# Kernel tuning notes

Hardware: AMD Instinct MI355X
Metric: run time of the kernel (lower is better)

Reference implementation:

```python
import jax, jax.numpy as jnp
import numpy as np

B, T, D, H = 2, 2048, 2048, 16
HD = D // H  # head_dim = 128
NEG = -1e9


def setup_inputs() -> dict:
    key = jax.random.key(0)
    k1, k2, k3 = jax.random.split(key, 3)
    x = jax.random.normal(k1, (B, T, D), dtype=jnp.float32)
    # additive causal mask: 0 on/below diagonal, large negative above
    mask = jnp.where(jnp.tril(jnp.ones((T, T), dtype=bool)), 0.0, NEG).astype(jnp.float32)
    causal_mask = mask[None, None]  # [1,1,T,T]
    w_qkv = jax.random.normal(k2, (3 * D, D), dtype=jnp.float32) * (D ** -0.5)
    w_out = jax.random.normal(k3, (D, D), dtype=jnp.float32) * (D ** -0.5)
    b_out = jnp.zeros((D,), dtype=jnp.float32)
    return {"x": x, "causal_mask": causal_mask, "w_qkv": w_qkv, "w_out": w_out, "b_out": b_out}


def reference(x, causal_mask, w_qkv, w_out, b_out):
    scale = HD ** -0.5
    qkv = jnp.einsum('btd,ed->bte', x, w_qkv)          # [B,T,3D]
    q, k, v = jnp.split(qkv, 3, axis=-1)
    def heads(t):  # [B,T,D] -> [B,H,T,HD]
        return t.reshape(B, T, H, HD).transpose(0, 2, 1, 3)
    q, k, v = heads(q), heads(k), heads(v)
    attn = jnp.einsum('bhqd,bhkd->bhqk', q, k) * scale + causal_mask
    attn = jax.nn.softmax(attn, axis=-1)
    out = jnp.einsum('bhqk,bhkd->bhqd', attn, v)       # [B,H,T,HD]
    out = out.transpose(0, 2, 1, 3).reshape(B, T, D)
    return jnp.einsum('btd,ed->bte', out, w_out) + b_out
```

## Files before the change

### kernel.cpp

```cpp
#include <hip/hip_runtime.h>
#include <stdint.h>

typedef uint16_t u16;
typedef __attribute__((ext_vector_type(8))) short short8;
typedef __attribute__((ext_vector_type(4))) float f32x4;
typedef __attribute__((ext_vector_type(16))) float f32x16;

#define MFMA16(a, b, c) __builtin_amdgcn_mfma_f32_16x16x32_bf16((a), (b), (c), 0, 0, 0)
#define MFMA32(a, b, c) __builtin_amdgcn_mfma_f32_32x32x16_bf16((a), (b), (c), 0, 0, 0)
#define AS1 __attribute__((address_space(1)))
#define AS3 __attribute__((address_space(3)))

__device__ __forceinline__ void gld_lds16(const u16* g, u16* l) {
  __builtin_amdgcn_global_load_lds((const AS1 void*)g, (AS3 void*)l, 16, 0, 0);
}

__device__ __forceinline__ u16 f2bf(float f) {
  uint32_t u = __float_as_uint(f);
  u += 0x7fffu + ((u >> 16) & 1u);
  return (u16)(u >> 16);
}

__global__ __launch_bounds__(256) void cvt_all(const float* __restrict__ x,
                                               const float* __restrict__ wqkv,
                                               const float* __restrict__ wout,
                                               u16* __restrict__ xb,
                                               u16* __restrict__ wqkvb,
                                               u16* __restrict__ woutb) {
  const int n1 = 8388608 / 4, n2 = 12582912 / 4;
  int i = blockIdx.x * 256 + threadIdx.x;
  const float* src;
  u16* dst;
  int j;
  if (i < n1) {
    src = x; dst = xb; j = i;
  } else if (i < n1 + n2) {
    src = wqkv; dst = wqkvb; j = i - n1;
  } else {
    src = wout; dst = woutb; j = i - n1 - n2;
  }
  float4 v = ((const float4*)src)[j];
  uint2 o;
  o.x = (uint32_t)f2bf(v.x) | ((uint32_t)f2bf(v.y) << 16);
  o.y = (uint32_t)f2bf(v.z) | ((uint32_t)f2bf(v.w) << 16);
  ((uint2*)dst)[j] = o;
}

template <int N>
__device__ __forceinline__ void bar_vm() {
  asm volatile("s_waitcnt vmcnt(%0)\n\ts_barrier" ::"n"(N) : "memory");
}

template <int MFR>
__device__ __forceinline__ void gemm_core3(const u16* __restrict__ Ab,
                                           const u16* __restrict__ Bb,
                                           u16* sm, int tid,
                                           f32x4 acc[MFR][4]) {
  constexpr int AROWS = MFR * 32;
  constexpr int ASZ = AROWS * 32;
  constexpr int BSZ = 128 * 32;
  constexpr int BUF = ASZ + BSZ;
  constexpr int NT = 64;
  constexpr int ALD = AROWS / 64;
  constexpr int VN = ALD + 2;

  const int lane = tid & 63, w = tid >> 6;
  const int wr = w >> 1, wc = w & 1;
  const int lo = lane & 15, q4 = lane >> 4;
  const int pcl = (((lo & 1) << 2) | q4) ^ ((lo >> 1) & 7);
  const int loff = (lo >> 1) * 64 + pcl * 8;

  auto stage = [&](int g) {
    u16* As = sm + (g % 3) * BUF;
    u16* Bs = As + ASZ;
    const int k0 = g * 32;
#pragma unroll
    for (int s = 0; s < ALD; ++s) {
      const int c = tid + s * 256;
      const int sr = c >> 3, pc = c & 7;
      const int t = pc ^ (sr & 7);
      const int r = sr * 2 + (t >> 2), c4 = t & 3;
      gld_lds16(Ab + (size_t)r * 2048 + k0 + c4 * 8, As + c * 8);
    }
#pragma unroll
    for (int s = 0; s < 2; ++s) {
      const int c = tid + s * 256;
      const int sr = c >> 3, pc = c & 7;
      const int t = pc ^ (sr & 7);
      const int r = sr * 2 + (t >> 2), c4 = t & 3;
      gld_lds16(Bb + (size_t)r * 2048 + k0 + c4 * 8, Bs + c * 8);
    }
  };

  stage(0);
  stage(1);
  bar_vm<VN>();

  for (int g = 0; g < NT; ++g) {
    const u16* As = sm + (g % 3) * BUF;
    const u16* Bs = As + ASZ;
    if (g + 2 < NT) stage(g + 2);
    short8 af[MFR], bf[4];
#pragma unroll
    for (int i = 0; i < MFR; ++i)
      af[i] = *(const short8*)(As + (wr * (MFR * 16) + i * 16) * 32 + loff);
#pragma unroll
    for (int j = 0; j < 4; ++j)
      bf[j] = *(const short8*)(Bs + (wc * 64 + j * 16) * 32 + loff);
    __builtin_amdgcn_s_setprio(1);
#pragma unroll
    for (int i = 0; i < MFR; ++i)
#pragma unroll
      for (int j = 0; j < 4; ++j) acc[i][j] = MFMA16(af[i], bf[j], acc[i][j]);
    __builtin_amdgcn_s_setprio(0);
    if (g + 1 < NT) {
      if (g + 2 < NT) {
        bar_vm<VN>();
      } else {
        bar_vm<0>();
      }
    }
  }
}

__global__ __launch_bounds__(256, 2) void proj_gemm(const u16* __restrict__ xb,
                                                    const u16* __restrict__ wqkvb,
                                                    u16* __restrict__ qkb,
                                                    u16* __restrict__ vtb) {
  __shared__ u16 sm[3 * (256 * 32 + 128 * 32)];
  const int tid = threadIdx.x;
  const int lane = tid & 63, w = tid >> 6;
  const int wr = w >> 1, wc = w & 1;
  const int lo = lane & 15, q4 = lane >> 4;

  if (blockIdx.x < 512) {
    int bx = blockIdx.x;
    bx = (bx & 7) * 64 + (bx >> 3);
    const int mt = bx >> 5, nt = bx & 31;
    const u16* Ab = xb + (size_t)mt * 256 * 2048;
    const u16* Bb = wqkvb + (size_t)nt * 128 * 2048;
    u16* C = qkb + (size_t)mt * 256 * 4096 + nt * 128;
    f32x4 acc[8][4];
    const f32x4 fzero = {0.f, 0.f, 0.f, 0.f};
#pragma unroll
    for (int i = 0; i < 8; ++i)
#pragma unroll
      for (int j = 0; j < 4; ++j) acc[i][j] = fzero;
    gemm_core3<8>(Ab, Bb, sm, tid, acc);
#pragma unroll
    for (int i = 0; i < 8; ++i)
#pragma unroll
      for (int j = 0; j < 4; ++j) {
        const int col = wc * 64 + j * 16 + lo;
#pragma unroll
        for (int e = 0; e < 4; ++e) {
          const int row = wr * 128 + i * 16 + q4 * 4 + e;
          C[(size_t)row * 4096 + col] = f2bf(acc[i][j][e]);
        }
      }
  } else {
    int idx = blockIdx.x - 512;
    idx = (idx & 7) * 64 + (idx >> 3);
    const int mt = idx >> 5, nt = idx & 31;
    const u16* Ab = wqkvb + (size_t)(4096 + mt * 128) * 2048;
    const u16* Bb = xb + (size_t)nt * 128 * 2048;
    u16* C = vtb + (size_t)mt * 128 * 4096 + nt * 128;
    f32x4 acc[4][4];
    const f32x4 fzero = {0.f, 0.f, 0.f, 0.f};
#pragma unroll
    for (int i = 0; i < 4; ++i)
#pragma unroll
      for (int j = 0; j < 4; ++j) acc[i][j] = fzero;
    gemm_core3<4>(Ab, Bb, sm, tid, acc);
#pragma unroll
    for (int i = 0; i < 4; ++i)
#pragma unroll
      for (int j = 0; j < 4; ++j) {
        const int col = wc * 64 + j * 16 + lo;
#pragma unroll
        for (int e = 0; e < 4; ++e) {
          const int row = wr * 64 + i * 16 + q4 * 4 + e;
          C[(size_t)row * 4096 + col] = f2bf(acc[i][j][e]);
        }
      }
  }
}

__global__ __launch_bounds__(256, 2) void out_gemm(const u16* __restrict__ A,
                                                   const u16* __restrict__ B,
                                                   float* __restrict__ Cf,
                                                   const float* __restrict__ bias) {
  __shared__ u16 sm[3 * (256 * 32 + 128 * 32)];
  int bx = blockIdx.x;
  bx = (bx & 7) * 32 + (bx >> 3);
  const int tid = threadIdx.x;
  const int mt = bx >> 4, nt = bx & 15;
  const u16* Ab = A + (size_t)mt * 256 * 2048;
  const u16* Bb = B + (size_t)nt * 128 * 2048;
  f32x4 acc[8][4];
  const f32x4 fzero = {0.f, 0.f, 0.f, 0.f};
#pragma unroll
  for (int i = 0; i < 8; ++i)
#pragma unroll
    for (int j = 0; j < 4; ++j) acc[i][j] = fzero;

  gemm_core3<8>(Ab, Bb, sm, tid, acc);

  const int lane = tid & 63, w = tid >> 6;
  const int wr = w >> 1, wc = w & 1;
  const int lo = lane & 15, q4 = lane >> 4;
#pragma unroll
  for (int i = 0; i < 8; ++i)
#pragma unroll
    for (int j = 0; j < 4; ++j) {
      const int col = nt * 128 + wc * 64 + j * 16 + lo;
      const float bv = bias[col];
#pragma unroll
      for (int e = 0; e < 4; ++e) {
        const int row = mt * 256 + wr * 128 + i * 16 + q4 * 4 + e;
        Cf[(size_t)row * 2048 + col] = acc[i][j][e] + bv;
      }
    }
}

__device__ __forceinline__ int swz(int r, int c) {
  return r * 128 + (c ^ (((r ^ (r >> 3)) & 7) << 4));
}

__global__ __launch_bounds__(512) void flash_attn(const u16* __restrict__ qk,
                                                  const u16* __restrict__ vt,
                                                  u16* __restrict__ aout) {
  constexpr int T = 2048, WQK = 4096, D = 2048;
  constexpr int TILE = 128 * 128;
  __shared__ u16 smem[5 * TILE];

  const int bx = blockIdx.x;
  const int p = bx >> 5;
  const int g = bx & 31;
  const int h = g & 15, b = g >> 4;
  const int tid = threadIdx.x, lane = tid & 63, w = tid >> 6;
  const int wr = w >> 1, wcc = w & 1;
  const int l31 = lane & 31, h5 = lane >> 5;

  const u16* Qb = qk + (size_t)b * T * WQK + h * 128;
  const u16* Kb = Qb + 2048;
  const u16* Vtb = vt + (size_t)h * 128 * 4096 + b * 2048;
  u16* Ps = smem + 4 * TILE;

  const float cexp = 0.08838834764831843f * 1.4426950408889634f;
  short8 onesf;
#pragma unroll
  for (int j = 0; j < 8; ++j) onesf[j] = (short)0x3F80;

  for (int half = 0; half < 2; ++half) {
    const int qt = half ? p : 15 - p;
    const int q0 = qt * 128;

    short8 qf[8];
#pragma unroll
    for (int kc = 0; kc < 8; ++kc)
      qf[kc] = *(const short8*)(Qb + (size_t)(q0 + wr * 32 + l31) * WQK +
                                kc * 16 + h5 * 8);

    f32x16 o[2], osum;
#pragma unroll
    for (int e = 0; e < 16; ++e) { o[0][e] = 0.f; o[1][e] = 0.f; osum[e] = 0.f; }

    __syncthreads();
#pragma unroll
    for (int s = 0; s < 4; ++s) {
      const int c = tid + s * 512, r = c >> 4, cc = c & 15;
      const int cs = cc ^ (((r ^ (r >> 3)) & 7) << 1);
      gld_lds16(Kb + (size_t)r * WQK + cs * 8, smem + c * 8);
      gld_lds16(Vtb + (size_t)r * 4096 + cs * 8, smem + 2 * TILE + c * 8);
    }

    for (int kt = 0; kt <= qt; ++kt) {
      const int curo = (kt & 1) * TILE, nxto = TILE - curo;
      __syncthreads();
      if (kt < qt) {
        const int k0n = (kt + 1) * 128;
#pragma unroll
        for (int s = 0; s < 4; ++s) {
          const int c = tid + s * 512, r = c >> 4, cc = c & 15;
          const int cs = cc ^ (((r ^ (r >> 3)) & 7) << 1);
          gld_lds16(Kb + (size_t)(k0n + r) * WQK + cs * 8, smem + nxto + c * 8);
          gld_lds16(Vtb + (size_t)r * 4096 + k0n + cs * 8,
                    smem + 2 * TILE + nxto + c * 8);
        }
      }

      const u16* Ksc = smem + curo;
      const u16* Vsc = smem + 2 * TILE + curo;

      f32x16 s2[2];
#pragma unroll
      for (int e = 0; e < 16; ++e) { s2[0][e] = 0.f; s2[1][e] = 0.f; }
#pragma unroll
      for (int kc = 0; kc < 8; ++kc)
#pragma unroll
        for (int ct = 0; ct < 2; ++ct) {
          short8 kf = *(const short8*)&Ksc[swz(wcc * 64 + ct * 32 + l31,
                                               kc * 16 + h5 * 8)];
          s2[ct] = MFMA32(qf[kc], kf, s2[ct]);
        }

      const bool diag = (kt == qt);
#pragma unroll
      for (int ct = 0; ct < 2; ++ct) {
        const int kcol = wcc * 64 + ct * 32 + l31;
#pragma unroll
        for (int reg = 0; reg < 16; ++reg) {
          const int qrow = wr * 32 + (reg & 3) + 8 * (reg >> 2) + 4 * h5;
          float pv = exp2f(s2[ct][reg] * cexp);
          if (diag && (kcol > qrow)) pv = 0.f;
          Ps[swz(qrow, kcol)] = f2bf(pv);
        }
      }
      asm volatile("s_waitcnt lgkmcnt(0)\n\ts_barrier" ::: "memory");

#pragma unroll
      for (int kc = 0; kc < 8; ++kc) {
        short8 pa = *(const short8*)&Ps[swz(wr * 32 + l31, kc * 16 + h5 * 8)];
        osum = MFMA32(pa, onesf, osum);
#pragma unroll
        for (int dt = 0; dt < 2; ++dt) {
          short8 vf = *(const short8*)&Vsc[swz(wcc * 64 + dt * 32 + l31,
                                               kc * 16 + h5 * 8)];
          o[dt] = MFMA32(pa, vf, o[dt]);
        }
      }
    }

#pragma unroll
    for (int reg = 0; reg < 16; ++reg) {
      const int row = q0 + wr * 32 + (reg & 3) + 8 * (reg >> 2) + 4 * h5;
      const float inv = 1.f / osum[reg];
#pragma unroll
      for (int dt = 0; dt < 2; ++dt)
        aout[(size_t)(b * T + row) * D + h * 128 + wcc * 64 + dt * 32 + l31] =
            f2bf(o[dt][reg] * inv);
    }
  }
}

extern "C" void kernel_launch(void* const* d_in, const int* in_sizes, int n_in,
                              void* d_out, int out_size, void* d_ws, size_t ws_size,
                              hipStream_t stream) {
  const float* x = (const float*)d_in[0];
  const float* w_qkv = (const float*)d_in[2];
  const float* w_out = (const float*)d_in[3];
  const float* b_out = (const float*)d_in[4];
  float* out = (float*)d_out;

  const int BT = 4096, D = 2048, D3 = 6144;
  u16* xb = (u16*)d_ws;
  u16* wqkvb = xb + (size_t)BT * D;
  u16* woutb = wqkvb + (size_t)D3 * D;
  u16* qkb = woutb + (size_t)D * D;
  u16* vtb = qkb + (size_t)BT * 4096;
  u16* attnb = vtb + (size_t)D * BT;

  const int total4 = (BT * D + D3 * D + D * D) / 4;
  cvt_all<<<total4 / 256, 256, 0, stream>>>(x, w_qkv, w_out, xb, wqkvb, woutb);
  proj_gemm<<<1024, 256, 0, stream>>>(xb, wqkvb, qkb, vtb);
  flash_attn<<<256, 512, 0, stream>>>(qkb, vtb, attnb);
  out_gemm<<<256, 256, 0, stream>>>(attnb, woutb, out, b_out);
}
```

Measured before the change: 366.4 us.

## Split QKV projection into 8-wave 256x256 QK GEMM and separate 256-row V GEMM

Replaces the single combined projection kernel with two launches. The Q/K part uses a new 512-thread kernel with 256x256 output tiles, a K-step of 64, double-buffered LDS and quarter-by-quarter interleaved staging of the next tile alongside the MFMAs. The V-transpose part now uses 256-row tiles in its own launch. The aim is more reuse per loaded byte and better overlap of loads with compute. The cost is an extra kernel launch and a more intricate barrier/vmcnt schedule that must be exactly right.

```diff
diff --git a/kernel.cpp b/kernel.cpp
--- a/kernel.cpp
+++ b/kernel.cpp
@@ -50,6 +50,118 @@
 __device__ __forceinline__ void bar_vm() {
   asm volatile("s_waitcnt vmcnt(%0)\n\ts_barrier" ::"n"(N) : "memory");
 }
+__device__ __forceinline__ void bar_fence() {
+  asm volatile("s_barrier" ::: "memory");
+}
+
+__global__ __launch_bounds__(512, 2) void proj8_gemm(const u16* __restrict__ xb,
+                                                     const u16* __restrict__ wqkvb,
+                                                     u16* __restrict__ qkb) {
+  constexpr int ASZ = 256 * 64;
+  constexpr int NT = 32;
+  __shared__ u16 sm[4 * ASZ];
+
+  int bx = blockIdx.x;
+  bx = (bx & 7) * 32 + (bx >> 3);
+  const int mt = bx >> 4, nt = bx & 15;
+  const u16* Ab = xb + (size_t)mt * 256 * 2048;
+  const u16* Bb = wqkvb + (size_t)nt * 256 * 2048;
+  u16* C = qkb + (size_t)mt * 256 * 4096 + nt * 256;
+
+  const int tid = threadIdx.x, lane = tid & 63, w = tid >> 6;
+  const int wm = w >> 2, wn = w & 3;
+  const int lo = lane & 15, q4 = lane >> 4;
+
+  f32x4 acc[8][4];
+  const f32x4 fzero = {0.f, 0.f, 0.f, 0.f};
+#pragma unroll
+  for (int i = 0; i < 8; ++i)
+#pragma unroll
+    for (int j = 0; j < 4; ++j) acc[i][j] = fzero;
+
+  auto stage_half = [&](int tau, int h) {
+    const int slot = tau & 1;
+    const int k0 = tau * 64;
+    const u16* G = (h < 2) ? Bb : Ab;
+    u16* L = sm + (h < 2 ? 2 * ASZ : 0) + slot * ASZ;
+#pragma unroll
+    for (int s = 0; s < 2; ++s) {
+      const int c = tid + s * 512;
+      const int hr = c >> 3, pc = c & 7;
+      const int r = (h < 2) ? (h * 128 + hr)
+                            : ((hr & 63) + ((hr >> 6) << 7) + ((h & 1) << 6));
+      const int c4 = pc ^ (r & 7);
+      gld_lds16(G + (size_t)r * 2048 + k0 + c4 * 8, L + r * 64 + pc * 8);
+    }
+  };
+
+  stage_half(0, 0);
+  stage_half(0, 1);
+  stage_half(0, 2);
+  stage_half(0, 3);
+  bar_vm<2>();
+
+  for (int tau = 0; tau < NT; ++tau) {
+    const u16* As = sm + (tau & 1) * ASZ;
+    const u16* Bs = sm + 2 * ASZ + (tau & 1) * ASZ;
+    short8 bf[8];
+#pragma unroll
+    for (int q = 0; q < 4; ++q) {
+      if (q == 0) {
+#pragma unroll
+        for (int j = 0; j < 4; ++j)
+#pragma unroll
+          for (int kk = 0; kk < 2; ++kk) {
+            const int r = wn * 64 + j * 16 + lo;
+            bf[j * 2 + kk] =
+                *(const short8*)(Bs + r * 64 + (((kk * 4 + q4) ^ (r & 7)) * 8));
+          }
+      }
+      short8 af[2][2];
+#pragma unroll
+      for (int i = 0; i < 2; ++i)
+#pragma unroll
+        for (int kk = 0; kk < 2; ++kk) {
+          const int r = wm * 128 + q * 32 + i * 16 + lo;
+          af[i][kk] =
+              *(const short8*)(As + r * 64 + (((kk * 4 + q4) ^ (r & 7)) * 8));
+        }
+      if (tau + 1 < NT) stage_half(tau + 1, q);
+      bar_fence();
+      __builtin_amdgcn_s_setprio(1);
+#pragma unroll
+      for (int i = 0; i < 2; ++i)
+#pragma unroll
+        for (int j = 0; j < 4; ++j)
+#pragma unroll
+          for (int kk = 0; kk < 2; ++kk)
+            acc[q * 2 + i][j] = MFMA16(af[i][kk], bf[j * 2 + kk], acc[q * 2 + i][j]);
+      __builtin_amdgcn_s_setprio(0);
+      if (q == 0) {
+        if (tau == NT - 1) bar_vm<0>();
+        else bar_vm<2>();
+      } else if (q == 1) {
+        bar_vm<4>();
+      } else if (q == 2) {
+        bar_vm<6>();
+      } else {
+        if (tau < NT - 1) bar_vm<2>();
+      }
+    }
+  }
+
+#pragma unroll
+  for (int i = 0; i < 8; ++i)
+#pragma unroll
+    for (int j = 0; j < 4; ++j) {
+      const int col = wn * 64 + j * 16 + lo;
+#pragma unroll
+      for (int e = 0; e < 4; ++e) {
+        const int row = wm * 128 + i * 16 + q4 * 4 + e;
+        C[(size_t)row * 4096 + col] = f2bf(acc[i][j][e]);
+      }
+    }
+}
 
 template <int MFR>
 __device__ __forceinline__ void gemm_core3(const u16* __restrict__ Ab,
@@ -123,67 +235,40 @@
   }
 }
 
-__global__ __launch_bounds__(256, 2) void proj_gemm(const u16* __restrict__ xb,
-                                                    const u16* __restrict__ wqkvb,
-                                                    u16* __restrict__ qkb,
-                                                    u16* __restrict__ vtb) {
+__global__ __launch_bounds__(256, 2) void vproj_gemm(const u16* __restrict__ wqkvb,
+                                                     const u16* __restrict__ xb,
+                                                     u16* __restrict__ vtb) {
   __shared__ u16 sm[3 * (256 * 32 + 128 * 32)];
+  int bx = blockIdx.x;
+  bx = (bx & 7) * 32 + (bx >> 3);
   const int tid = threadIdx.x;
+  const int mt = bx >> 5, nt = bx & 31;
+  const u16* Ab = wqkvb + (size_t)(4096 + mt * 256) * 2048;
+  const u16* Bb = xb + (size_t)nt * 128 * 2048;
+  u16* C = vtb + (size_t)mt * 256 * 4096 + nt * 128;
+  f32x4 acc[8][4];
+  const f32x4 fzero = {0.f, 0.f, 0.f, 0.f};
+#pragma unroll
+  for (int i = 0; i < 8; ++i)
+#pragma unroll
+    for (int j = 0; j < 4; ++j) acc[i][j] = fzero;
+
+  gemm_core3<8>(Ab, Bb, sm, tid, acc);
+
   const int lane = tid & 63, w = tid >> 6;
   const int wr = w >> 1, wc = w & 1;
   const int lo = lane & 15, q4 = lane >> 4;
-
-  if (blockIdx.x < 512) {
-    int bx = blockIdx.x;
-    bx = (bx & 7) * 64 + (bx >> 3);
-    const int mt = bx >> 5, nt = bx & 31;
-    const u16* Ab = xb + (size_t)mt * 256 * 2048;
-    const u16* Bb = wqkvb + (size_t)nt * 128 * 2048;
-    u16* C = qkb + (size_t)mt * 256 * 4096 + nt * 128;
-    f32x4 acc[8][4];
-    const f32x4 fzero = {0.f, 0.f, 0.f, 0.f};
-#pragma unroll
-    for (int i = 0; i < 8; ++i)
-#pragma unroll
-      for (int j = 0; j < 4; ++j) acc[i][j] = fzero;
-    gemm_core3<8>(Ab, Bb, sm, tid, acc);
-#pragma unroll
-    for (int i = 0; i < 8; ++i)
-#pragma unroll
-      for (int j = 0; j < 4; ++j) {
-        const int col = wc * 64 + j * 16 + lo;
-#pragma unroll
-        for (int e = 0; e < 4; ++e) {
-          const int row = wr * 128 + i * 16 + q4 * 4 + e;
-          C[(size_t)row * 4096 + col] = f2bf(acc[i][j][e]);
-        }
-      }
-  } else {
-    int idx = blockIdx.x - 512;
-    idx = (idx & 7) * 64 + (idx >> 3);
-    const int mt = idx >> 5, nt = idx & 31;
-    const u16* Ab = wqkvb + (size_t)(4096 + mt * 128) * 2048;
-    const u16* Bb = xb + (size_t)nt * 128 * 2048;
-    u16* C = vtb + (size_t)mt * 128 * 4096 + nt * 128;
-    f32x4 acc[4][4];
-    const f32x4 fzero = {0.f, 0.f, 0.f, 0.f};
-#pragma unroll
-    for (int i = 0; i < 4; ++i)
-#pragma unroll
-      for (int j = 0; j < 4; ++j) acc[i][j] = fzero;
-    gemm_core3<4>(Ab, Bb, sm, tid, acc);
-#pragma unroll
-    for (int i = 0; i < 4; ++i)
-#pragma unroll
-      for (int j = 0; j < 4; ++j) {
-        const int col = wc * 64 + j * 16 + lo;
-#pragma unroll
-        for (int e = 0; e < 4; ++e) {
-          const int row = wr * 64 + i * 16 + q4 * 4 + e;
-          C[(size_t)row * 4096 + col] = f2bf(acc[i][j][e]);
-        }
-      }
-  }
+#pragma unroll
+  for (int i = 0; i < 8; ++i)
+#pragma unroll
+    for (int j = 0; j < 4; ++j) {
+      const int col = wc * 64 + j * 16 + lo;
+#pragma unroll
+      for (int e = 0; e < 4; ++e) {
+        const int row = wr * 128 + i * 16 + q4 * 4 + e;
+        C[(size_t)row * 4096 + col] = f2bf(acc[i][j][e]);
+      }
+    }
 }
 
 __global__ __launch_bounds__(256, 2) void out_gemm(const u16* __restrict__ A,
@@ -363,7 +448,8 @@
 
   const int total4 = (BT * D + D3 * D + D * D) / 4;
   cvt_all<<<total4 / 256, 256, 0, stream>>>(x, w_qkv, w_out, xb, wqkvb, woutb);
-  proj_gemm<<<1024, 256, 0, stream>>>(xb, wqkvb, qkb, vtb);
+  proj8_gemm<<<256, 512, 0, stream>>>(xb, wqkvb, qkb);
+  vproj_gemm<<<256, 256, 0, stream>>>(wqkvb, xb, vtb);
   flash_attn<<<256, 512, 0, stream>>>(qkb, vtb, attnb);
   out_gemm<<<256, 256, 0, stream>>>(attnb, woutb, out, b_out);
 }
```

After: 355.9 us. -2.9%, faster.
